# Kernel optimization log

Hardware: AMD Instinct MI355X
Metric: run time of the kernel (lower is better)

The kernel has to match this reference:

```python
import jax, jax.numpy as jnp
import numpy as np

L = 3
NUM_KERNELS = 16
BATCH = 128   # conv in/out channels (torch 'batch_size')
SLIDE = 256   # slide_len, acts as conv batch dim
D = 128       # embedding width, equals conv kernel width


def setup_inputs() -> dict:
    key = jax.random.key(0)
    ks = jax.random.split(key, 7)
    # number of kernels per height h=1,2,3 for idx % 3 pattern over 16 kernels
    counts = [len(range(h, NUM_KERNELS, L)) for h in range(L)]  # [6, 5, 5]
    inp = {
        "Ec": jax.random.normal(ks[0], (BATCH, SLIDE, L, D), dtype=jnp.float32),
        "W1": jax.random.normal(ks[1], (counts[0], BATCH, BATCH, 1, D), dtype=jnp.float32) * 0.05,
        "W2": jax.random.normal(ks[2], (counts[1], BATCH, BATCH, 2, D), dtype=jnp.float32) * 0.05,
        "W3": jax.random.normal(ks[3], (counts[2], BATCH, BATCH, 3, D), dtype=jnp.float32) * 0.05,
        "b1": jax.random.normal(ks[4], (counts[0], BATCH), dtype=jnp.float32) * 0.05,
        "b2": jax.random.normal(ks[5], (counts[1], BATCH), dtype=jnp.float32) * 0.05,
        "b3": jax.random.normal(ks[6], (counts[2], BATCH), dtype=jnp.float32) * 0.05,
    }
    return inp


def reference(Ec, W1, W2, W3, b1, b2, b3):
    # Ec: (B, S, L, d) -> transpose to (S, B, L, d); S is the conv batch dim,
    # B is the channel dim (Conv2d(batch_size, batch_size, (h, d))).
    Ec_t = jnp.transpose(Ec, (1, 0, 2, 3))  # (S, B, L, d)
    Ws = [W1, W2, W3]
    bs = [b1, b2, b3]
    res = [None] * NUM_KERNELS  # each entry: (S, B)
    for h_idx in range(L):
        h = h_idx + 1
        P = L - h + 1  # conv output height == maxpool window
        idxs = list(range(h_idx, NUM_KERNELS, L))  # kernels with this height
        # windows: (P, S, B, h, d) -- the P valid vertical positions
        windows = jnp.stack([Ec_t[:, :, p:p + h, :] for p in range(P)], axis=0)
        # conv over (channel, h, d): (P, k, S, out_channel=B)
        conv = jnp.einsum('pscad,kocad->pkso', windows, Ws[h_idx])
        conv = conv + bs[h_idx][None, :, None, :]
        # maxpool over the P positions, then ReLU
        pooled = jax.nn.relu(jnp.max(conv, axis=0))  # (k, S, B)
        for j, idx in enumerate(idxs):
            res[idx] = pooled[j]
    out = jnp.stack(res, axis=-1)  # (S, B, K)
    # torch: (S,B,K,1) -> transpose(0,1) -> transpose(-1,-2) => (B, S, 1, K)
    return jnp.transpose(out, (1, 0, 2))[:, :, None, :]
```

## Files before the change

kernel.cpp:

```cpp
#include <hip/hip_runtime.h>
#include <hip/hip_bf16.h>

#define NBATCH 128
#define NSLIDE 256
#define NDEMB  128
#define NSLOT  33
#define CCHUNKS 8
#define CPER    (NBATCH / CCHUNKS)
#define KCHUNK  (CPER * NDEMB)
#define BM 128
#define BN 128
#define BK 32
#define NIT (KCHUNK / BK)
#define LDK (BK + 8)
#define CONV_ELEMS (NSLOT * NSLIDE * NBATCH)

using ushort8 = __attribute__((ext_vector_type(8))) unsigned short;
using bf16x8  = __attribute__((ext_vector_type(8))) __bf16;
using floatx4 = __attribute__((ext_vector_type(4))) float;

__device__ __constant__ unsigned char U_L[53] = {
  0,0,0,0,0,0,0,0,0,0,0,0,0,0,0,0,
  1,1,1,1,1,1,1,1,1,1,1,1,1,1,1,1,1,1,1,1,1,
  2,2,2,2,2,2,2,2,2,2,2,2,2,2,2,2};
__device__ __constant__ unsigned char U_H[53] = {
  0,0,0,0,0,0, 1,1,1,1,1, 2,2,2,2,2,
  0,0,0,0,0,0, 1,1,1,1,1, 1,1,1,1,1, 2,2,2,2,2,
  0,0,0,0,0,0, 1,1,1,1,1, 2,2,2,2,2};
__device__ __constant__ unsigned char U_K[53] = {
  0,1,2,3,4,5, 0,1,2,3,4, 0,1,2,3,4,
  0,1,2,3,4,5, 0,1,2,3,4, 0,1,2,3,4, 0,1,2,3,4,
  0,1,2,3,4,5, 0,1,2,3,4, 0,1,2,3,4};
__device__ __constant__ unsigned char U_A[53] = {
  0,0,0,0,0,0, 0,0,0,0,0, 0,0,0,0,0,
  0,0,0,0,0,0, 1,1,1,1,1, 0,0,0,0,0, 1,1,1,1,1,
  0,0,0,0,0,0, 1,1,1,1,1, 2,2,2,2,2};
__device__ __constant__ unsigned char U_SLOT[53] = {
  0,3,6,9,12,15, 18,20,22,24,26, 28,29,30,31,32,
  1,4,7,10,13,16, 18,20,22,24,26, 19,21,23,25,27, 28,29,30,31,32,
  2,5,8,11,14,17, 19,21,23,25,27, 28,29,30,31,32};

__device__ __forceinline__ unsigned short f2bf(float f) {
  union { float f; unsigned u; } v; v.f = f;
  unsigned r = v.u + 0x7fffu + ((v.u >> 16) & 1u);
  return (unsigned short)(r >> 16);
}

__global__ void zero_ws(float* __restrict__ p) {
  int i = blockIdx.x * 256 + threadIdx.x;
  reinterpret_cast<float4*>(p)[i] = make_float4(0.f, 0.f, 0.f, 0.f);
}

__global__ __launch_bounds__(256, 2) void gemm_units(
    const float* __restrict__ Ec,
    const float* __restrict__ W1, const float* __restrict__ W2,
    const float* __restrict__ W3,
    float* __restrict__ conv)
{
  const int bx     = blockIdx.x;
  const int cc     = blockIdx.y;
  const int unit   = bx >> 1;
  const int m_half = bx & 1;

  const int l     = U_L[unit];
  const int h_idx = U_H[unit];
  const int kker  = U_K[unit];
  const int aa    = U_A[unit];
  const int slot  = U_SLOT[unit];
  const int h     = h_idx + 1;

  const float* wbase = (h_idx == 0) ? W1 : ((h_idx == 1) ? W2 : W3);
  const long o_stride = 16384L * h;
  const long c_stride = 128L * h;
  const float* wp = wbase + (long)kker * (128L * o_stride) + (long)aa * 128;
  const int c0 = cc * CPER;

  __shared__ __align__(16) unsigned short As[BM][LDK];
  __shared__ __align__(16) unsigned short Bs[BN][LDK];

  const int tid   = threadIdx.x;
  const int srow  = tid >> 1;
  const int shalf = (tid & 1) * 16;

  const float* aBase = Ec + (long)l * 128 + (long)(m_half * 128 + srow) * 384 + shalf;
  const float* wBase = wp + (long)srow * o_stride + shalf;

  const int wave = tid >> 6;
  const int lane = tid & 63;
  const int wm = (wave >> 1) * 64;
  const int wn = (wave & 1) * 64;
  const int lr = lane & 15;
  const int lq = lane >> 4;

  floatx4 acc[4][4];
#pragma unroll
  for (int i = 0; i < 4; ++i)
#pragma unroll
    for (int j = 0; j < 4; ++j) acc[i][j] = (floatx4){0.f, 0.f, 0.f, 0.f};

  float4 aL[4], wL[4];
  {
    const int c = c0;
    const float4* ap4 = reinterpret_cast<const float4*>(aBase + (long)c * 98304);
    const float4* wp4 = reinterpret_cast<const float4*>(wBase + (long)c * c_stride);
#pragma unroll
    for (int q = 0; q < 4; ++q) { aL[q] = ap4[q]; wL[q] = wp4[q]; }
  }

  for (int it = 0; it < NIT; ++it) {
    __syncthreads();
    {
      ushort8 pa0 = { f2bf(aL[0].x), f2bf(aL[0].y), f2bf(aL[0].z), f2bf(aL[0].w),
                      f2bf(aL[1].x), f2bf(aL[1].y), f2bf(aL[1].z), f2bf(aL[1].w) };
      ushort8 pa1 = { f2bf(aL[2].x), f2bf(aL[2].y), f2bf(aL[2].z), f2bf(aL[2].w),
                      f2bf(aL[3].x), f2bf(aL[3].y), f2bf(aL[3].z), f2bf(aL[3].w) };
      ushort8 pw0 = { f2bf(wL[0].x), f2bf(wL[0].y), f2bf(wL[0].z), f2bf(wL[0].w),
                      f2bf(wL[1].x), f2bf(wL[1].y), f2bf(wL[1].z), f2bf(wL[1].w) };
      ushort8 pw1 = { f2bf(wL[2].x), f2bf(wL[2].y), f2bf(wL[2].z), f2bf(wL[2].w),
                      f2bf(wL[3].x), f2bf(wL[3].y), f2bf(wL[3].z), f2bf(wL[3].w) };
      *reinterpret_cast<ushort8*>(&As[srow][shalf])     = pa0;
      *reinterpret_cast<ushort8*>(&As[srow][shalf + 8]) = pa1;
      *reinterpret_cast<ushort8*>(&Bs[srow][shalf])     = pw0;
      *reinterpret_cast<ushort8*>(&Bs[srow][shalf + 8]) = pw1;
    }
    __syncthreads();

    if (it + 1 < NIT) {
      const int kk0 = (it + 1) * BK;
      const int c = c0 + (kk0 >> 7);
      const int d0 = kk0 & 127;
      const float4* ap4 = reinterpret_cast<const float4*>(aBase + (long)c * 98304 + d0);
      const float4* wp4 = reinterpret_cast<const float4*>(wBase + (long)c * c_stride + d0);
#pragma unroll
      for (int q = 0; q < 4; ++q) { aL[q] = ap4[q]; wL[q] = wp4[q]; }
    }

    bf16x8 af[4], bf_[4];
#pragma unroll
    for (int i = 0; i < 4; ++i)
      af[i] = *reinterpret_cast<const bf16x8*>(&As[wm + 16 * i + lr][lq * 8]);
#pragma unroll
    for (int j = 0; j < 4; ++j)
      bf_[j] = *reinterpret_cast<const bf16x8*>(&Bs[wn + 16 * j + lr][lq * 8]);
#pragma unroll
    for (int i = 0; i < 4; ++i)
#pragma unroll
      for (int j = 0; j < 4; ++j)
        acc[i][j] = __builtin_amdgcn_mfma_f32_16x16x32_bf16(af[i], bf_[j], acc[i][j], 0, 0, 0);
  }

  float* cslot = conv + (long)slot * (NSLIDE * NBATCH);
#pragma unroll
  for (int i = 0; i < 4; ++i) {
#pragma unroll
    for (int j = 0; j < 4; ++j) {
#pragma unroll
      for (int r = 0; r < 4; ++r) {
        int s = m_half * 128 + wm + 16 * i + lq * 4 + r;
        int o = wn + 16 * j + lr;
        atomicAdd(&cslot[s * NBATCH + o], acc[i][j][r]);
      }
    }
  }
}

__global__ void epilogue(const float* __restrict__ conv,
                         const float* __restrict__ b1, const float* __restrict__ b2,
                         const float* __restrict__ b3, float* __restrict__ out)
{
  int t = blockIdx.x * 256 + threadIdx.x;
  int o = t & 127;
  int s = t >> 7;
  const float* base = conv + s * NBATCH + o;
  float r[16];
#pragma unroll
  for (int k = 0; k < 6; ++k) {
    float m = base[(3 * k + 0) * 32768];
    m = fmaxf(m, base[(3 * k + 1) * 32768]);
    m = fmaxf(m, base[(3 * k + 2) * 32768]);
    r[3 * k + 0] = fmaxf(m + b1[k * 128 + o], 0.f);
  }
#pragma unroll
  for (int k = 0; k < 5; ++k) {
    float m = fmaxf(base[(18 + 2 * k) * 32768], base[(18 + 2 * k + 1) * 32768]);
    r[3 * k + 1] = fmaxf(m + b2[k * 128 + o], 0.f);
  }
#pragma unroll
  for (int k = 0; k < 5; ++k) {
    r[3 * k + 2] = fmaxf(base[(28 + k) * 32768] + b3[k * 128 + o], 0.f);
  }
  float* op = out + ((long)o * 256 + s) * 16;
  reinterpret_cast<float4*>(op)[0] = make_float4(r[0], r[1], r[2], r[3]);
  reinterpret_cast<float4*>(op)[1] = make_float4(r[4], r[5], r[6], r[7]);
  reinterpret_cast<float4*>(op)[2] = make_float4(r[8], r[9], r[10], r[11]);
  reinterpret_cast<float4*>(op)[3] = make_float4(r[12], r[13], r[14], r[15]);
}

extern "C" void kernel_launch(void* const* d_in, const int* in_sizes, int n_in,
                              void* d_out, int out_size, void* d_ws, size_t ws_size,
                              hipStream_t stream) {
  const float* Ec = (const float*)d_in[0];
  const float* W1 = (const float*)d_in[1];
  const float* W2 = (const float*)d_in[2];
  const float* W3 = (const float*)d_in[3];
  const float* b1 = (const float*)d_in[4];
  const float* b2 = (const float*)d_in[5];
  const float* b3 = (const float*)d_in[6];
  float* out  = (float*)d_out;
  float* conv = (float*)d_ws;

  zero_ws<<<CONV_ELEMS / 4 / 256, 256, 0, stream>>>(conv);
  gemm_units<<<dim3(106, CCHUNKS), 256, 0, stream>>>(Ec, W1, W2, W3, conv);
  epilogue<<<(NSLIDE * NBATCH) / 256, 256, 0, stream>>>(conv, b1, b2, b3, out);
}
```

Measured before the change: 467.4 us.

## Restructure conv GEMM per output slot with swizzled LDS and partial-sum buffers

Reorganizes the work so each block computes one full output slot (kernel, position) and loops over all h rows of the filter, instead of one (row, filter-row) unit accumulated via atomics. K tiles grow to 64 with an XOR-swizzled LDS layout that avoids bank conflicts, and per-channel-chunk partials are written with plain stores to a separate buffer and reduced in the epilogue. This removes the zero-init kernel and the float atomics. In exchange the epilogue must read 8x more data, and the workspace grows to 8 copies of the conv buffer.

```diff
diff --git a/kernel.cpp b/kernel.cpp
--- a/kernel.cpp
+++ b/kernel.cpp
@@ -3,42 +3,34 @@
 
 #define NBATCH 128
 #define NSLIDE 256
-#define NDEMB  128
 #define NSLOT  33
 #define CCHUNKS 8
-#define CPER    (NBATCH / CCHUNKS)
-#define KCHUNK  (CPER * NDEMB)
-#define BM 128
-#define BN 128
-#define BK 32
-#define NIT (KCHUNK / BK)
-#define LDK (BK + 8)
-#define CONV_ELEMS (NSLOT * NSLIDE * NBATCH)
+#define CPER    16
+#define BK      64
+#define NIT     ((CPER * 128) / BK)
+#define SLOT_ELEMS (NSLIDE * NBATCH)
+#define CC_STRIDE  (NSLOT * SLOT_ELEMS)
 
 using ushort8 = __attribute__((ext_vector_type(8))) unsigned short;
 using bf16x8  = __attribute__((ext_vector_type(8))) __bf16;
 using floatx4 = __attribute__((ext_vector_type(4))) float;
 
-__device__ __constant__ unsigned char U_L[53] = {
-  0,0,0,0,0,0,0,0,0,0,0,0,0,0,0,0,
-  1,1,1,1,1,1,1,1,1,1,1,1,1,1,1,1,1,1,1,1,1,
-  2,2,2,2,2,2,2,2,2,2,2,2,2,2,2,2};
-__device__ __constant__ unsigned char U_H[53] = {
-  0,0,0,0,0,0, 1,1,1,1,1, 2,2,2,2,2,
-  0,0,0,0,0,0, 1,1,1,1,1, 1,1,1,1,1, 2,2,2,2,2,
-  0,0,0,0,0,0, 1,1,1,1,1, 2,2,2,2,2};
-__device__ __constant__ unsigned char U_K[53] = {
-  0,1,2,3,4,5, 0,1,2,3,4, 0,1,2,3,4,
-  0,1,2,3,4,5, 0,1,2,3,4, 0,1,2,3,4, 0,1,2,3,4,
-  0,1,2,3,4,5, 0,1,2,3,4, 0,1,2,3,4};
-__device__ __constant__ unsigned char U_A[53] = {
-  0,0,0,0,0,0, 0,0,0,0,0, 0,0,0,0,0,
-  0,0,0,0,0,0, 1,1,1,1,1, 0,0,0,0,0, 1,1,1,1,1,
-  0,0,0,0,0,0, 1,1,1,1,1, 2,2,2,2,2};
-__device__ __constant__ unsigned char U_SLOT[53] = {
-  0,3,6,9,12,15, 18,20,22,24,26, 28,29,30,31,32,
-  1,4,7,10,13,16, 18,20,22,24,26, 19,21,23,25,27, 28,29,30,31,32,
-  2,5,8,11,14,17, 19,21,23,25,27, 28,29,30,31,32};
+__device__ __constant__ unsigned char S_H[NSLOT] = {
+  2,2,2,2,2,
+  1,1,1,1,1,1,1,1,1,1,
+  0,0,0,0,0,0,0,0,0,0,0,0,0,0,0,0,0,0};
+__device__ __constant__ unsigned char S_K[NSLOT] = {
+  0,1,2,3,4,
+  0,0,1,1,2,2,3,3,4,4,
+  0,0,0,1,1,1,2,2,2,3,3,3,4,4,4,5,5,5};
+__device__ __constant__ unsigned char S_P[NSLOT] = {
+  0,0,0,0,0,
+  0,1,0,1,0,1,0,1,0,1,
+  0,1,2,0,1,2,0,1,2,0,1,2,0,1,2,0,1,2};
+__device__ __constant__ unsigned char S_SLOT[NSLOT] = {
+  28,29,30,31,32,
+  18,19,20,21,22,23,24,25,26,27,
+  0,1,2,3,4,5,6,7,8,9,10,11,12,13,14,15,16,17};
 
 __device__ __forceinline__ unsigned short f2bf(float f) {
   union { float f; unsigned u; } v; v.f = f;
@@ -46,44 +38,47 @@
   return (unsigned short)(r >> 16);
 }
 
-__global__ void zero_ws(float* __restrict__ p) {
-  int i = blockIdx.x * 256 + threadIdx.x;
-  reinterpret_cast<float4*>(p)[i] = make_float4(0.f, 0.f, 0.f, 0.f);
-}
-
-__global__ __launch_bounds__(256, 2) void gemm_units(
+__device__ __forceinline__ ushort8 pack8(const float4& a, const float4& b) {
+  ushort8 p = { f2bf(a.x), f2bf(a.y), f2bf(a.z), f2bf(a.w),
+                f2bf(b.x), f2bf(b.y), f2bf(b.z), f2bf(b.w) };
+  return p;
+}
+
+__global__ __launch_bounds__(256, 2) void gemm_slots(
     const float* __restrict__ Ec,
     const float* __restrict__ W1, const float* __restrict__ W2,
     const float* __restrict__ W3,
-    float* __restrict__ conv)
+    float* __restrict__ part)
 {
   const int bx     = blockIdx.x;
   const int cc     = blockIdx.y;
-  const int unit   = bx >> 1;
+  const int sidx   = bx >> 1;
   const int m_half = bx & 1;
 
-  const int l     = U_L[unit];
-  const int h_idx = U_H[unit];
-  const int kker  = U_K[unit];
-  const int aa    = U_A[unit];
-  const int slot  = U_SLOT[unit];
+  const int h_idx = S_H[sidx];
+  const int kker  = S_K[sidx];
+  const int p     = S_P[sidx];
+  const int slot  = S_SLOT[sidx];
   const int h     = h_idx + 1;
 
   const float* wbase = (h_idx == 0) ? W1 : ((h_idx == 1) ? W2 : W3);
   const long o_stride = 16384L * h;
   const long c_stride = 128L * h;
-  const float* wp = wbase + (long)kker * (128L * o_stride) + (long)aa * 128;
+  const float* wk = wbase + (long)kker * (128L * o_stride);
   const int c0 = cc * CPER;
-
-  __shared__ __align__(16) unsigned short As[BM][LDK];
-  __shared__ __align__(16) unsigned short Bs[BN][LDK];
-
-  const int tid   = threadIdx.x;
-  const int srow  = tid >> 1;
-  const int shalf = (tid & 1) * 16;
-
-  const float* aBase = Ec + (long)l * 128 + (long)(m_half * 128 + srow) * 384 + shalf;
-  const float* wBase = wp + (long)srow * o_stride + shalf;
+  const int NT = h * NIT;
+
+  __shared__ __align__(16) unsigned short As[128 * 64];
+  __shared__ __align__(16) unsigned short Bs[128 * 64];
+
+  const int tid = threadIdx.x;
+  const int c8  = tid & 7;
+  const int rb  = tid >> 3;
+  const int swz = ((c8 ^ (rb & 7)) << 3);
+
+  const float* aP = Ec + (long)p * 128 + (long)(m_half * 128 + rb) * 384
+                    + c8 * 8 + (long)c0 * 98304;
+  const float* wP = wk + (long)rb * o_stride + c8 * 8 + (long)c0 * c_stride;
 
   const int wave = tid >> 6;
   const int lane = tid & 63;
@@ -98,58 +93,67 @@
 #pragma unroll
     for (int j = 0; j < 4; ++j) acc[i][j] = (floatx4){0.f, 0.f, 0.f, 0.f};
 
-  float4 aL[4], wL[4];
-  {
-    const int c = c0;
-    const float4* ap4 = reinterpret_cast<const float4*>(aBase + (long)c * 98304);
-    const float4* wp4 = reinterpret_cast<const float4*>(wBase + (long)c * c_stride);
-#pragma unroll
-    for (int q = 0; q < 4; ++q) { aL[q] = ap4[q]; wL[q] = wp4[q]; }
-  }
-
-  for (int it = 0; it < NIT; ++it) {
-    __syncthreads();
-    {
-      ushort8 pa0 = { f2bf(aL[0].x), f2bf(aL[0].y), f2bf(aL[0].z), f2bf(aL[0].w),
-                      f2bf(aL[1].x), f2bf(aL[1].y), f2bf(aL[1].z), f2bf(aL[1].w) };
-      ushort8 pa1 = { f2bf(aL[2].x), f2bf(aL[2].y), f2bf(aL[2].z), f2bf(aL[2].w),
-                      f2bf(aL[3].x), f2bf(aL[3].y), f2bf(aL[3].z), f2bf(aL[3].w) };
-      ushort8 pw0 = { f2bf(wL[0].x), f2bf(wL[0].y), f2bf(wL[0].z), f2bf(wL[0].w),
-                      f2bf(wL[1].x), f2bf(wL[1].y), f2bf(wL[1].z), f2bf(wL[1].w) };
-      ushort8 pw1 = { f2bf(wL[2].x), f2bf(wL[2].y), f2bf(wL[2].z), f2bf(wL[2].w),
-                      f2bf(wL[3].x), f2bf(wL[3].y), f2bf(wL[3].z), f2bf(wL[3].w) };
-      *reinterpret_cast<ushort8*>(&As[srow][shalf])     = pa0;
-      *reinterpret_cast<ushort8*>(&As[srow][shalf + 8]) = pa1;
-      *reinterpret_cast<ushort8*>(&Bs[srow][shalf])     = pw0;
-      *reinterpret_cast<ushort8*>(&Bs[srow][shalf + 8]) = pw1;
+  float4 aL[8], wL[8];
+
+#define LOAD_TILE(t_)                                                           \
+  {                                                                             \
+    const int tv  = (t_);                                                       \
+    const int av  = tv >> 5;                                                    \
+    const int itv = tv & 31;                                                    \
+    const long aOff = (long)av * 128 + (long)(itv >> 1) * 98304                 \
+                      + (long)(itv & 1) * 64;                                   \
+    const long bOff = (long)av * 128 + (long)(itv >> 1) * c_stride              \
+                      + (long)(itv & 1) * 64;                                   \
+    _Pragma("unroll")                                                           \
+    for (int q = 0; q < 4; ++q) {                                               \
+      const float* ap = aP + aOff + (long)q * (32 * 384);                       \
+      const float* bp = wP + bOff + (long)q * 32 * o_stride;                    \
+      aL[2 * q]     = *reinterpret_cast<const float4*>(ap);                     \
+      aL[2 * q + 1] = *reinterpret_cast<const float4*>(ap + 4);                 \
+      wL[2 * q]     = *reinterpret_cast<const float4*>(bp);                     \
+      wL[2 * q + 1] = *reinterpret_cast<const float4*>(bp + 4);                 \
+    }                                                                           \
+  }
+
+  LOAD_TILE(0);
+
+  for (int t = 0; t < NT; ++t) {
+#pragma unroll
+    for (int q = 0; q < 4; ++q) {
+      const int row = rb + 32 * q;
+      *reinterpret_cast<ushort8*>(&As[row * 64 + swz]) = pack8(aL[2*q], aL[2*q+1]);
+      *reinterpret_cast<ushort8*>(&Bs[row * 64 + swz]) = pack8(wL[2*q], wL[2*q+1]);
     }
     __syncthreads();
 
-    if (it + 1 < NIT) {
-      const int kk0 = (it + 1) * BK;
-      const int c = c0 + (kk0 >> 7);
-      const int d0 = kk0 & 127;
-      const float4* ap4 = reinterpret_cast<const float4*>(aBase + (long)c * 98304 + d0);
-      const float4* wp4 = reinterpret_cast<const float4*>(wBase + (long)c * c_stride + d0);
-#pragma unroll
-      for (int q = 0; q < 4; ++q) { aL[q] = ap4[q]; wL[q] = wp4[q]; }
+    if (t + 1 < NT) LOAD_TILE(t + 1);
+
+#pragma unroll
+    for (int ks = 0; ks < 2; ++ks) {
+      bf16x8 af[4], bf_[4];
+#pragma unroll
+      for (int i = 0; i < 4; ++i) {
+        const int row = wm + 16 * i + lr;
+        const int col = (((ks * 4 + lq) ^ (lr & 7)) << 3);
+        af[i] = *reinterpret_cast<const bf16x8*>(&As[row * 64 + col]);
+      }
+#pragma unroll
+      for (int j = 0; j < 4; ++j) {
+        const int row = wn + 16 * j + lr;
+        const int col = (((ks * 4 + lq) ^ (lr & 7)) << 3);
+        bf_[j] = *reinterpret_cast<const bf16x8*>(&Bs[row * 64 + col]);
+      }
+#pragma unroll
+      for (int i = 0; i < 4; ++i)
+#pragma unroll
+        for (int j = 0; j < 4; ++j)
+          acc[i][j] = __builtin_amdgcn_mfma_f32_16x16x32_bf16(af[i], bf_[j], acc[i][j], 0, 0, 0);
     }
-
-    bf16x8 af[4], bf_[4];
-#pragma unroll
-    for (int i = 0; i < 4; ++i)
-      af[i] = *reinterpret_cast<const bf16x8*>(&As[wm + 16 * i + lr][lq * 8]);
-#pragma unroll
-    for (int j = 0; j < 4; ++j)
-      bf_[j] = *reinterpret_cast<const bf16x8*>(&Bs[wn + 16 * j + lr][lq * 8]);
-#pragma unroll
-    for (int i = 0; i < 4; ++i)
-#pragma unroll
-      for (int j = 0; j < 4; ++j)
-        acc[i][j] = __builtin_amdgcn_mfma_f32_16x16x32_bf16(af[i], bf_[j], acc[i][j], 0, 0, 0);
-  }
-
-  float* cslot = conv + (long)slot * (NSLIDE * NBATCH);
+    __syncthreads();
+  }
+#undef LOAD_TILE
+
+  float* base = part + ((long)cc * NSLOT + slot) * SLOT_ELEMS;
 #pragma unroll
   for (int i = 0; i < 4; ++i) {
 #pragma unroll
@@ -158,36 +162,45 @@
       for (int r = 0; r < 4; ++r) {
         int s = m_half * 128 + wm + 16 * i + lq * 4 + r;
         int o = wn + 16 * j + lr;
-        atomicAdd(&cslot[s * NBATCH + o], acc[i][j][r]);
+        base[s * NBATCH + o] = acc[i][j][r];
       }
     }
   }
 }
 
-__global__ void epilogue(const float* __restrict__ conv,
+__global__ void epilogue(const float* __restrict__ part,
                          const float* __restrict__ b1, const float* __restrict__ b2,
                          const float* __restrict__ b3, float* __restrict__ out)
 {
   int t = blockIdx.x * 256 + threadIdx.x;
   int o = t & 127;
   int s = t >> 7;
-  const float* base = conv + s * NBATCH + o;
+  const float* base = part + s * NBATCH + o;
+
+  float v[NSLOT];
+#pragma unroll
+  for (int sl = 0; sl < NSLOT; ++sl) {
+    float a = 0.f;
+#pragma unroll
+    for (int cc = 0; cc < CCHUNKS; ++cc)
+      a += base[(long)cc * CC_STRIDE + sl * SLOT_ELEMS];
+    v[sl] = a;
+  }
+
   float r[16];
 #pragma unroll
   for (int k = 0; k < 6; ++k) {
-    float m = base[(3 * k + 0) * 32768];
-    m = fmaxf(m, base[(3 * k + 1) * 32768]);
-    m = fmaxf(m, base[(3 * k + 2) * 32768]);
+    float m = fmaxf(fmaxf(v[3 * k + 0], v[3 * k + 1]), v[3 * k + 2]);
     r[3 * k + 0] = fmaxf(m + b1[k * 128 + o], 0.f);
   }
 #pragma unroll
   for (int k = 0; k < 5; ++k) {
-    float m = fmaxf(base[(18 + 2 * k) * 32768], base[(18 + 2 * k + 1) * 32768]);
+    float m = fmaxf(v[18 + 2 * k], v[18 + 2 * k + 1]);
     r[3 * k + 1] = fmaxf(m + b2[k * 128 + o], 0.f);
   }
 #pragma unroll
   for (int k = 0; k < 5; ++k) {
-    r[3 * k + 2] = fmaxf(base[(28 + k) * 32768] + b3[k * 128 + o], 0.f);
+    r[3 * k + 2] = fmaxf(v[28 + k] + b3[k * 128 + o], 0.f);
   }
   float* op = out + ((long)o * 256 + s) * 16;
   reinterpret_cast<float4*>(op)[0] = make_float4(r[0], r[1], r[2], r[3]);
@@ -207,9 +220,8 @@
   const float* b2 = (const float*)d_in[5];
   const float* b3 = (const float*)d_in[6];
   float* out  = (float*)d_out;
-  float* conv = (float*)d_ws;
-
-  zero_ws<<<CONV_ELEMS / 4 / 256, 256, 0, stream>>>(conv);
-  gemm_units<<<dim3(106, CCHUNKS), 256, 0, stream>>>(Ec, W1, W2, W3, conv);
-  epilogue<<<(NSLIDE * NBATCH) / 256, 256, 0, stream>>>(conv, b1, b2, b3, out);
-}
+  float* part = (float*)d_ws;
+
+  gemm_slots<<<dim3(66, CCHUNKS), 256, 0, stream>>>(Ec, W1, W2, W3, part);
+  epilogue<<<(NSLIDE * NBATCH) / 256, 256, 0, stream>>>(part, b1, b2, b3, out);
+}
```

Result: slower. 659.2 us (+41.0%).
